# Performance work log

Measured on AMD Instinct MI355X. Metric: run time of the kernel, lower is better.

Reference implementation:

```python
import jax, jax.numpy as jnp
import numpy as np

F_FIELDS, HH, WW = 17, 300, 400   # hardcoded cifhr buffer in __init__
H_F, W_F = 38, 50                 # field grid: ~hr_size / stride
STRIDE = 8
V_TH = 0.1
NEIGHBORS = 16
MIN_SCALE = 0.0
FACTOR = 1.0
R = 13                            # window half-width; covers 2*sigma_max = 12 truncation radius


def _approx_exp(x):
    # openpifpaf fast exp approximation; only evaluated for x in [-2, 0]
    y = 1.0 + x / 8.0
    y = y * y
    y = y * y
    y = y * y
    return y


def _accumulate(cifhr, field):
    # field: (F, 5, H_f, W_f) with channels [confidence, x_reg, y_reg, b, scale]
    F = field.shape[0]
    v = field[:, 0]                        # (F,H,W)
    px = field[:, 1] * STRIDE              # hr-grid x position
    py = field[:, 2] * STRIDE              # hr-grid y position
    scale = field[:, 4]
    sigma = jnp.maximum(1.0, 0.5 * scale * STRIDE)
    value = v / NEIGHBORS * FACTOR
    valid = (v >= V_TH) & (scale * STRIDE >= MIN_SCALE)

    cx = jnp.round(px).astype(jnp.int32)
    cy = jnp.round(py).astype(jnp.int32)
    offs = jnp.arange(-R, R + 1, dtype=jnp.int32)   # (K,)
    xx = cx[..., None] + offs                        # (F,H,W,K)
    yy = cy[..., None] + offs                        # (F,H,W,K)
    dx2 = (xx.astype(px.dtype) - px[..., None]) ** 2  # (F,H,W,K)
    dy2 = (yy.astype(py.dtype) - py[..., None]) ** 2  # (F,H,W,K)
    d2 = dy2[..., :, None] + dx2[..., None, :]       # (F,H,W,K,K) y-major
    sigma2 = (sigma ** 2)[..., None, None]
    trunc2 = 4.0 * sigma2                            # truncate = 2*sigma
    inb = ((yy >= 0) & (yy < HH))[..., :, None] & ((xx >= 0) & (xx < WW))[..., None, :]
    mask = (d2 <= trunc2) & inb & valid[..., None, None]
    nearest = (dy2[..., :, None] < 0.25) & (dx2[..., None, :] < 0.25)
    g = jnp.where(nearest, 1.0, _approx_exp(-0.5 * d2 / sigma2))
    contrib = jnp.where(mask, value[..., None, None] * g, 0.0)

    fidx = jnp.arange(F, dtype=jnp.int32)[:, None, None, None, None]
    yc = jnp.clip(yy[..., :, None], 0, HH - 1)
    xc = jnp.clip(xx[..., None, :], 0, WW - 1)
    flat_idx = (fidx * HH + yc) * WW + xc            # (F,H,W,K,K)
    out = cifhr.reshape(-1).at[flat_idx.reshape(-1)].add(contrib.reshape(-1))
    return jnp.minimum(out.reshape(F_FIELDS, HH, WW), 1.0)


def setup_inputs() -> dict:
    key = jax.random.key(0)
    k1, k2, k3, k4, k5 = jax.random.split(key, 5)
    cifhr = jnp.zeros((F_FIELDS, HH, WW), dtype=jnp.float32)
    # confidence in [0,1]
    conf = jax.random.uniform(k1, (F_FIELDS, 1, H_F, W_F), dtype=jnp.float32)
    gx = jnp.broadcast_to(jnp.arange(W_F, dtype=jnp.float32)[None, None, None, :],
                          (F_FIELDS, 1, H_F, W_F))
    gy = jnp.broadcast_to(jnp.arange(H_F, dtype=jnp.float32)[None, None, :, None],
                          (F_FIELDS, 1, H_F, W_F))
    xr = gx + 0.5 * jax.random.normal(k2, (F_FIELDS, 1, H_F, W_F), dtype=jnp.float32)
    yr = gy + 0.5 * jax.random.normal(k3, (F_FIELDS, 1, H_F, W_F), dtype=jnp.float32)
    b = jax.random.uniform(k4, (F_FIELDS, 1, H_F, W_F), dtype=jnp.float32)
    # scale in [0.5, 1.5] -> sigma = max(1, 0.5*scale*stride) <= 6
    scale = 0.5 + jax.random.uniform(k5, (F_FIELDS, 1, H_F, W_F), dtype=jnp.float32)
    x = jnp.concatenate([conf, xr, yr, b, scale], axis=1)  # (17,5,38,50)
    return {"cifhr": cifhr, "x": x}


def reference(cifhr, x):
    return _accumulate(cifhr, x)
```

## Files before the change

### kernel.cpp

```cpp
#include <hip/hip_runtime.h>
#include <stdint.h>

#define F_FIELDS 17
#define HH 300
#define WW 400
#define H_F 38
#define W_F 50
#define PTS_PER_FIELD (H_F * W_F)
#define RAD 13

#define GX 13
#define GY 10
#define CAP 64

#define NB 16

__device__ __forceinline__ float bcast(float v, int k) {
    return __int_as_float(__builtin_amdgcn_readlane(__float_as_int(v), k));
}

__global__ __launch_bounds__(256) void cifhr_fused_kernel(
    const float* __restrict__ x, const float* __restrict__ cifhr,
    float* __restrict__ out) {
    __shared__ float4 sA[4][CAP];
    __shared__ float  sB[4][CAP];
    __shared__ int    cnt[4];

    const int tid = threadIdx.x;
    const int f = blockIdx.z;
    const int X0 = blockIdx.x * 32;
    const int Y0 = blockIdx.y * 32;
    const int sxmax = min(1, (WW - 1 - X0) >> 4);
    const int symax = min(1, (HH - 1 - Y0) >> 4);
    const int xvhi = X0 + ((sxmax + 1) << 4) - 1;
    const int yvhi = Y0 + ((symax + 1) << 4) - 1;

    if (tid < 4) cnt[tid] = 0;
    __syncthreads();

    const float* base = x + (size_t)(f * 5) * PTS_PER_FIELD;
    const int jlo = (X0 >> 3) - 6;
    const int ilo = (Y0 >> 3) - 6;
    const int i = ilo + (tid >> 4);
    const int j = jlo + (tid & 15);
    const bool ok = (i >= 0) & (i < H_F) & (j >= 0) & (j < W_F);
    const int p = ok ? (i * W_F + j) : 0;

    float v = 0.f, xr = 0.f, yr = 0.f, sc = 0.f;
    if (ok) {
        v  = base[p];
        xr = base[PTS_PER_FIELD + p];
        yr = base[2 * PTS_PER_FIELD + p];
        sc = base[4 * PTS_PER_FIELD + p];
    }
    if (ok && (v >= 0.1f) && (sc * 8.0f >= 0.0f)) {
        float px = xr * 8.0f;
        float py = yr * 8.0f;
        int cx = (int)rintf(px);
        int cy = (int)rintf(py);
        float sigma  = fmaxf(1.0f, 4.0f * sc);
        float sigma2 = sigma * sigma;
        int rp = min(RAD, (int)(2.0f * sigma + 0.5f));
        int xlo = cx - rp, xhi = cx + rp;
        int ylo = cy - rp, yhi = cy + rp;
        if (!(xhi < X0 || xlo > xvhi || yhi < Y0 || ylo > yvhi)) {
            int sx0 = max(0, (xlo - X0) >> 4), sx1 = min(sxmax, (xhi - X0) >> 4);
            int sy0 = max(0, (ylo - Y0) >> 4), sy1 = min(symax, (yhi - Y0) >> 4);
            float4 rec = make_float4(px, py, v * 0.0625f,
                                     -1.0f / (16.0f * sigma2));
            float tr = 4.0f * sigma2;
            for (int sy = sy0; sy <= sy1; ++sy)
                for (int sx = sx0; sx <= sx1; ++sx) {
                    int sidx = sy * 2 + sx;
                    int slot = atomicAdd(&cnt[sidx], 1);
                    if (slot < CAP) { sA[sidx][slot] = rec; sB[sidx][slot] = tr; }
                }
        }
    }
    __syncthreads();

    const int s  = tid >> 6, ln = tid & 63;
    const int sx = s & 1, sy = s >> 1;
    if (sx > sxmax || sy > symax) return;

    const int n = min(cnt[s], CAP);
    float4 mya = sA[s][ln];
    float  myt = sB[s][ln];

    const int xb = X0 + (sx << 4) + ((ln & 7) << 1);
    const int yb = Y0 + (sy << 4) + ((ln >> 3) << 1);
    const float xf0 = (float)xb, xf1 = (float)(xb + 1);
    const float yf0 = (float)yb, yf1 = (float)(yb + 1);

    const bool w0 = (yb < HH), w1 = (yb + 1 < HH);
    const size_t idx0 = ((size_t)f * HH + yb) * WW + xb;
    const size_t idx1 = idx0 + WW;
    float2 c0 = w0 ? *(const float2*)(cifhr + idx0) : make_float2(0.f, 0.f);
    float2 c1 = w1 ? *(const float2*)(cifhr + idx1) : make_float2(0.f, 0.f);

    float a00 = 0.0f, a01 = 0.0f, a10 = 0.0f, a11 = 0.0f;
    for (int k = 0; k < n; ++k) {
        float ax = bcast(mya.x, k);
        float ay = bcast(mya.y, k);
        float az = bcast(mya.z, k);
        float aw = bcast(mya.w, k);
        float tr = bcast(myt,   k);
        float dx0 = xf0 - ax, dx1 = xf1 - ax;
        float dy0 = yf0 - ay, dy1 = yf1 - ay;
        float dx0s = dx0 * dx0, dx1s = dx1 * dx1;
        float dy0s = dy0 * dy0, dy1s = dy1 * dy1;
        {   float d2 = dy0s + dx0s;
            float t8 = fmaf(aw, d2, 1.0f); t8 *= t8; t8 *= t8; t8 *= t8;
            float g  = (fmaxf(dy0s, dx0s) < 0.25f) ? 1.0f : t8;
            a00 += (d2 <= tr) ? az * g : 0.0f; }
        {   float d2 = dy0s + dx1s;
            float t8 = fmaf(aw, d2, 1.0f); t8 *= t8; t8 *= t8; t8 *= t8;
            float g  = (fmaxf(dy0s, dx1s) < 0.25f) ? 1.0f : t8;
            a01 += (d2 <= tr) ? az * g : 0.0f; }
        {   float d2 = dy1s + dx0s;
            float t8 = fmaf(aw, d2, 1.0f); t8 *= t8; t8 *= t8; t8 *= t8;
            float g  = (fmaxf(dy1s, dx0s) < 0.25f) ? 1.0f : t8;
            a10 += (d2 <= tr) ? az * g : 0.0f; }
        {   float d2 = dy1s + dx1s;
            float t8 = fmaf(aw, d2, 1.0f); t8 *= t8; t8 *= t8; t8 *= t8;
            float g  = (fmaxf(dy1s, dx1s) < 0.25f) ? 1.0f : t8;
            a11 += (d2 <= tr) ? az * g : 0.0f; }
    }

    if (w0) {
        float2 o; o.x = fminf(a00 + c0.x, 1.0f); o.y = fminf(a01 + c0.y, 1.0f);
        *(float2*)(out + idx0) = o;
    }
    if (w1) {
        float2 o; o.x = fminf(a10 + c1.x, 1.0f); o.y = fminf(a11 + c1.y, 1.0f);
        *(float2*)(out + idx1) = o;
    }
}

extern "C" void kernel_launch(void* const* d_in, const int* in_sizes, int n_in,
                              void* d_out, int out_size, void* d_ws, size_t ws_size,
                              hipStream_t stream) {
    const float* cifhr = (const float*)d_in[0];
    const float* x     = (const float*)d_in[1];
    float* out = (float*)d_out;

    dim3 grid(GX, GY, F_FIELDS);
    cifhr_fused_kernel<<<grid, 256, 0, stream>>>(x, cifhr, out);
}
```

Before: 74.89 us.

## Bin Gaussian sources into 8x8 subtiles and evaluate one pixel per lane

```diff
diff --git a/kernel.cpp b/kernel.cpp
--- a/kernel.cpp
+++ b/kernel.cpp
@@ -11,31 +11,27 @@
 
 #define GX 13
 #define GY 10
-#define CAP 64
+#define NT 16
+#define CAP 48
 
-#define NB 16
-
-__device__ __forceinline__ float bcast(float v, int k) {
-    return __int_as_float(__builtin_amdgcn_readlane(__float_as_int(v), k));
-}
 
 __global__ __launch_bounds__(256) void cifhr_fused_kernel(
     const float* __restrict__ x, const float* __restrict__ cifhr,
     float* __restrict__ out) {
-    __shared__ float4 sA[4][CAP];
-    __shared__ float  sB[4][CAP];
-    __shared__ int    cnt[4];
+    __shared__ float4 sA[NT][CAP];
+    __shared__ float  sB[NT][CAP];
+    __shared__ int    cnt[NT];
 
     const int tid = threadIdx.x;
-    const int f = blockIdx.z;
+    const int f  = blockIdx.z;
     const int X0 = blockIdx.x * 32;
     const int Y0 = blockIdx.y * 32;
-    const int sxmax = min(1, (WW - 1 - X0) >> 4);
-    const int symax = min(1, (HH - 1 - Y0) >> 4);
-    const int xvhi = X0 + ((sxmax + 1) << 4) - 1;
-    const int yvhi = Y0 + ((symax + 1) << 4) - 1;
+    const int xvhi = min(X0 + 31, WW - 1);
+    const int yvhi = min(Y0 + 31, HH - 1);
+    const int txmax = (xvhi - X0) >> 3;
+    const int tymax = (yvhi - Y0) >> 3;
 
-    if (tid < 4) cnt[tid] = 0;
+    if (tid < NT) cnt[tid] = 0;
     __syncthreads();
 
     const float* base = x + (size_t)(f * 5) * PTS_PER_FIELD;
@@ -64,16 +60,16 @@
         int xlo = cx - rp, xhi = cx + rp;
         int ylo = cy - rp, yhi = cy + rp;
         if (!(xhi < X0 || xlo > xvhi || yhi < Y0 || ylo > yvhi)) {
-            int sx0 = max(0, (xlo - X0) >> 4), sx1 = min(sxmax, (xhi - X0) >> 4);
-            int sy0 = max(0, (ylo - Y0) >> 4), sy1 = min(symax, (yhi - Y0) >> 4);
+            int tx0 = max(0, (xlo - X0) >> 3), tx1 = min(txmax, (xhi - X0) >> 3);
+            int ty0 = max(0, (ylo - Y0) >> 3), ty1 = min(tymax, (yhi - Y0) >> 3);
             float4 rec = make_float4(px, py, v * 0.0625f,
                                      -1.0f / (16.0f * sigma2));
             float tr = 4.0f * sigma2;
-            for (int sy = sy0; sy <= sy1; ++sy)
-                for (int sx = sx0; sx <= sx1; ++sx) {
-                    int sidx = sy * 2 + sx;
-                    int slot = atomicAdd(&cnt[sidx], 1);
-                    if (slot < CAP) { sA[sidx][slot] = rec; sB[sidx][slot] = tr; }
+            for (int ty = ty0; ty <= ty1; ++ty)
+                for (int tx = tx0; tx <= tx1; ++tx) {
+                    int t = ty * 4 + tx;
+                    int slot = atomicAdd(&cnt[t], 1);
+                    if (slot < CAP) { sA[t][slot] = rec; sB[t][slot] = tr; }
                 }
         }
     }
@@ -81,59 +77,37 @@
 
     const int s  = tid >> 6, ln = tid & 63;
     const int sx = s & 1, sy = s >> 1;
-    if (sx > sxmax || sy > symax) return;
+    const int lx = ln & 7, ly = ln >> 3;
 
-    const int n = min(cnt[s], CAP);
-    float4 mya = sA[s][ln];
-    float  myt = sB[s][ln];
+    #pragma unroll
+    for (int q = 0; q < 4; ++q) {
+        const int tX = (sx << 1) | (q & 1);
+        const int tY = (sy << 1) | (q >> 1);
+        if (tX > txmax || tY > tymax) continue;
+        const int t = tY * 4 + tX;
+        const int n = min(cnt[t], CAP);
 
-    const int xb = X0 + (sx << 4) + ((ln & 7) << 1);
-    const int yb = Y0 + (sy << 4) + ((ln >> 3) << 1);
-    const float xf0 = (float)xb, xf1 = (float)(xb + 1);
-    const float yf0 = (float)yb, yf1 = (float)(yb + 1);
+        const int xb = X0 + (tX << 3) + lx;
+        const int yb = Y0 + (tY << 3) + ly;
+        const bool wv = (yb < HH);
+        const size_t idx = ((size_t)f * HH + yb) * WW + xb;
+        const float c = wv ? cifhr[idx] : 0.0f;
+        const float xf = (float)xb, yf = (float)yb;
 
-    const bool w0 = (yb < HH), w1 = (yb + 1 < HH);
-    const size_t idx0 = ((size_t)f * HH + yb) * WW + xb;
-    const size_t idx1 = idx0 + WW;
-    float2 c0 = w0 ? *(const float2*)(cifhr + idx0) : make_float2(0.f, 0.f);
-    float2 c1 = w1 ? *(const float2*)(cifhr + idx1) : make_float2(0.f, 0.f);
-
-    float a00 = 0.0f, a01 = 0.0f, a10 = 0.0f, a11 = 0.0f;
-    for (int k = 0; k < n; ++k) {
-        float ax = bcast(mya.x, k);
-        float ay = bcast(mya.y, k);
-        float az = bcast(mya.z, k);
-        float aw = bcast(mya.w, k);
-        float tr = bcast(myt,   k);
-        float dx0 = xf0 - ax, dx1 = xf1 - ax;
-        float dy0 = yf0 - ay, dy1 = yf1 - ay;
-        float dx0s = dx0 * dx0, dx1s = dx1 * dx1;
-        float dy0s = dy0 * dy0, dy1s = dy1 * dy1;
-        {   float d2 = dy0s + dx0s;
-            float t8 = fmaf(aw, d2, 1.0f); t8 *= t8; t8 *= t8; t8 *= t8;
-            float g  = (fmaxf(dy0s, dx0s) < 0.25f) ? 1.0f : t8;
-            a00 += (d2 <= tr) ? az * g : 0.0f; }
-        {   float d2 = dy0s + dx1s;
-            float t8 = fmaf(aw, d2, 1.0f); t8 *= t8; t8 *= t8; t8 *= t8;
-            float g  = (fmaxf(dy0s, dx1s) < 0.25f) ? 1.0f : t8;
-            a01 += (d2 <= tr) ? az * g : 0.0f; }
-        {   float d2 = dy1s + dx0s;
-            float t8 = fmaf(aw, d2, 1.0f); t8 *= t8; t8 *= t8; t8 *= t8;
-            float g  = (fmaxf(dy1s, dx0s) < 0.25f) ? 1.0f : t8;
-            a10 += (d2 <= tr) ? az * g : 0.0f; }
-        {   float d2 = dy1s + dx1s;
-            float t8 = fmaf(aw, d2, 1.0f); t8 *= t8; t8 *= t8; t8 *= t8;
-            float g  = (fmaxf(dy1s, dx1s) < 0.25f) ? 1.0f : t8;
-            a11 += (d2 <= tr) ? az * g : 0.0f; }
-    }
-
-    if (w0) {
-        float2 o; o.x = fminf(a00 + c0.x, 1.0f); o.y = fminf(a01 + c0.y, 1.0f);
-        *(float2*)(out + idx0) = o;
-    }
-    if (w1) {
-        float2 o; o.x = fminf(a10 + c1.x, 1.0f); o.y = fminf(a11 + c1.y, 1.0f);
-        *(float2*)(out + idx1) = o;
+        float acc = 0.0f;
+        for (int k = 0; k < n; ++k) {
+            float4 a  = sA[t][k];
+            float  tr = sB[t][k];
+            float dx = xf - a.x, dy = yf - a.y;
+            float dx2 = dx * dx, dy2 = dy * dy;
+            float d2 = dy2 + dx2;
+            float u = fmaf(a.w, d2, 1.0f);
+            u *= u; u *= u; u *= u;
+            float g   = (fmaxf(dy2, dx2) < 0.25f) ? 1.0f : u;
+            float sel = (d2 <= tr) ? a.z : 0.0f;
+            acc = fmaf(sel, g, acc);
+        }
+        if (wv) out[idx] = fminf(acc + c, 1.0f);
     }
 }
 
@@ -142,8 +116,8 @@
                               hipStream_t stream) {
     const float* cifhr = (const float*)d_in[0];
     const float* x     = (const float*)d_in[1];
-    float* out = (float*)d_out;
+    float* outp = (float*)d_out;
 
     dim3 grid(GX, GY, F_FIELDS);
-    cifhr_fused_kernel<<<grid, 256, 0, stream>>>(x, cifhr, out);
+    cifhr_fused_kernel<<<grid, 256, 0, stream>>>(x, cifhr, outp);
 }
```

Result: no change. 73.55 us (-1.8%).
